# Kernel optimization log

Measured on AMD Instinct MI355X. Metric: run time of the kernel, lower is better.

Reference implementation:

```python
import jax, jax.numpy as jnp
import numpy as np

N, E, IN_DIM, OUT_DIM, SEM_DIM = 50000, 800000, 128, 128, 128
EPS = 1e-8


def setup_inputs() -> dict:
    key = jax.random.key(0)
    k = jax.random.split(key, 8)
    x = jax.random.normal(k[0], (N, IN_DIM), dtype=jnp.float32)
    edge_index = jax.random.randint(k[1], (2, E), 0, N, dtype=jnp.int64)
    semantic_vec = jax.random.normal(k[2], (N, SEM_DIM), dtype=jnp.float32)
    s = 1.0 / np.sqrt(IN_DIM)
    W_src = jax.random.uniform(k[3], (OUT_DIM, IN_DIM), jnp.float32, -s, s)
    b_src = jax.random.uniform(k[4], (OUT_DIM,), jnp.float32, -s, s)
    W_dst = jax.random.uniform(k[5], (OUT_DIM, IN_DIM), jnp.float32, -s, s)
    b_dst = jax.random.uniform(k[6], (OUT_DIM,), jnp.float32, -s, s)
    return {"x": x, "edge_index": edge_index, "semantic_vec": semantic_vec,
            "W_src": W_src, "b_src": b_src, "W_dst": W_dst, "b_dst": b_dst}


def _scatter_softmax(sim, dst, num_segments):
    # numerically stable segment-wise softmax over edges grouped by dst
    seg_max = jax.ops.segment_max(sim, dst, num_segments=num_segments)
    seg_max = jnp.where(jnp.isneginf(seg_max), 0.0, seg_max)
    e = jnp.exp(sim - seg_max[dst])
    seg_sum = jax.ops.segment_sum(e, dst, num_segments=num_segments)
    return e / (seg_sum[dst] + 1e-16)


def reference(x, edge_index, semantic_vec, W_src, b_src, W_dst, b_dst):
    src, dst = edge_index[0], edge_index[1]
    x_j = x[src] @ W_src.T + b_src           # [E, out_dim]
    # cosine similarity with torch eps semantics
    a = semantic_vec[src]
    b = semantic_vec[dst]
    na = jnp.maximum(jnp.linalg.norm(a, axis=-1), EPS)
    nb = jnp.maximum(jnp.linalg.norm(b, axis=-1), EPS)
    sim = jnp.sum(a * b, axis=-1) / (na * nb)  # [E]
    attn = _scatter_softmax(sim, dst, x.shape[0])
    msg = attn[:, None] * x_j                 # [E, out_dim]
    out = jax.ops.segment_sum(msg, dst, num_segments=x.shape[0])
    return out
```

## Files before the change

### kernel.cpp

```cpp
#include <hip/hip_runtime.h>
#include <hip/hip_fp16.h>

#define Nn 50000
#define Ee 800000
#define D  128
#define SLOT 64

#define B_SCAT 782
#define B_NORM 3125

struct h4 { __half2 lo, hi; };

typedef _Float16 f16x8 __attribute__((ext_vector_type(8)));
typedef float    f32x4 __attribute__((ext_vector_type(4)));

__global__ __launch_bounds__(256) void k_gemm(const float* __restrict__ x,
                                              const float* __restrict__ W,
                                              const float* __restrict__ b,
                                              __half* __restrict__ y16,
                                              int* __restrict__ cnt) {
  __shared__ __half sW16[128 * 136] __attribute__((aligned(16)));
  __shared__ __half sA16[64 * 136]  __attribute__((aligned(16)));
  int bid = blockIdx.x, tid = threadIdx.x;
  int n0 = bid * 64;

  if (tid < 16) {
    int idx = bid * 64 + tid * 4;
    *(int4*)(cnt + idx) = (int4){0, 0, 0, 0};
  }

  for (int r = 0; r < 16; r++) {
    int i = tid + 256 * r;
    int row = i >> 5, c4 = (i & 31) << 2;
    float4 w = *(const float4*)(W + (size_t)row * 128 + c4);
    __half2* dst = (__half2*)&sW16[row * 136 + c4];
    dst[0] = __floats2half2_rn(w.x, w.y);
    dst[1] = __floats2half2_rn(w.z, w.w);
  }
  for (int r = 0; r < 8; r++) {
    int i = tid + 256 * r;
    int row = i >> 5, c4 = (i & 31) << 2;
    int nr = n0 + row; if (nr >= Nn) nr = Nn - 1;
    float4 v = *(const float4*)(x + (size_t)nr * 128 + c4);
    __half2* dst = (__half2*)&sA16[row * 136 + c4];
    dst[0] = __floats2half2_rn(v.x, v.y);
    dst[1] = __floats2half2_rn(v.z, v.w);
  }
  __syncthreads();

  int wave = tid >> 6, lane = tid & 63;
  int g = lane >> 4, n16 = lane & 15;
  int m0 = n0 + wave * 16;

  f32x4 acc[8];
#pragma unroll
  for (int jt = 0; jt < 8; jt++) {
    float bias = b[jt * 16 + n16];
    acc[jt] = (f32x4){bias, bias, bias, bias};
  }

#pragma unroll
  for (int kt = 0; kt < 4; kt++) {
    f16x8 a = *(const f16x8*)(&sA16[(wave * 16 + n16) * 136 + kt * 32 + g * 8]);
#pragma unroll
    for (int jt = 0; jt < 8; jt++) {
      f16x8 bf = *(const f16x8*)(&sW16[(jt * 16 + n16) * 136 + kt * 32 + g * 8]);
      acc[jt] = __builtin_amdgcn_mfma_f32_16x16x32_f16(a, bf, acc[jt], 0, 0, 0);
    }
  }

#pragma unroll
  for (int jt = 0; jt < 8; jt++) {
#pragma unroll
    for (int r = 0; r < 4; r++) {
      int row = m0 + g * 4 + r;
      if (row < Nn)
        y16[(size_t)row * 128 + jt * 16 + n16] = __float2half(acc[jt][r]);
    }
  }
}

__global__ __launch_bounds__(256) void k_prep2(const int* __restrict__ ei,
                                               const float* __restrict__ sem,
                                               __half* __restrict__ sem16,
                                               int* __restrict__ cnt,
                                               unsigned short* __restrict__ slot16) {
  int bid = blockIdx.x, tid = threadIdx.x;
  if (bid < B_SCAT) {
    int base = bid * 1024 + tid;
#pragma unroll
    for (int u = 0; u < 4; u++) {
      int e = base + u * 256;
      if (e < Ee) {
        int s = ei[e], d = ei[Ee + e];
        int pos = atomicAdd(cnt + d, 1);
        if (pos < SLOT)
          slot16[(size_t)d * SLOT + pos] = (unsigned short)s;
      }
    }
  } else {
    int nb = (bid - B_SCAT) * 16;
    int wave = tid >> 6, lane = tid & 63;
#pragma unroll
    for (int it = 0; it < 4; it++) {
      int n = nb + it * 4 + wave;
      const float2 v = *(const float2*)(sem + (size_t)n * D + 2 * lane);
      float p = v.x * v.x + v.y * v.y;
#pragma unroll
      for (int off = 32; off > 0; off >>= 1) p += __shfl_xor(p, off);
      float inv = 1.0f / fmaxf(sqrtf(p), 1e-8f);
      *(__half2*)(sem16 + (size_t)n * D + 2 * lane) = __floats2half2_rn(v.x * inv, v.y * inv);
    }
  }
}

__global__ __launch_bounds__(256) void k_fused(const __half* __restrict__ sem16,
                                               const __half* __restrict__ y16,
                                               const unsigned short* __restrict__ slot16,
                                               const int* __restrict__ cnt,
                                               float* __restrict__ out) {
  int d = (blockIdx.x * 256 + threadIdx.x) >> 6;
  int lane = threadIdx.x & 63;
  if (d >= Nn) return;
  int sub = lane >> 5, l32 = lane & 31;
  int c = cnt[d]; if (c > SLOT) c = SLOT;

  int sv = (lane < c) ? (int)slot16[(size_t)d * SLOT + lane] : 0;

  h4 dref = ((const h4*)(sem16 + (size_t)d * D))[l32];
  float2 d0 = __half22float2(dref.lo), d1 = __half22float2(dref.hi);

  float Sp = 0.0f;
  float o0 = 0, o1 = 0, o2 = 0, o3 = 0;
  for (int i = 0; i < c; i += 4) {
    int ia = i + sub, ib = i + 2 + sub;
    int ca = ia < c ? ia : c - 1, cb = ib < c ? ib : c - 1;
    int sa = __shfl(sv, ca), sb = __shfl(sv, cb);
    h4 ra = ((const h4*)(sem16 + (size_t)sa * D))[l32];
    h4 rb = ((const h4*)(sem16 + (size_t)sb * D))[l32];
    h4 ya = ((const h4*)(y16 + (size_t)sa * D))[l32];
    h4 yb = ((const h4*)(y16 + (size_t)sb * D))[l32];
    float2 ra0 = __half22float2(ra.lo), ra1 = __half22float2(ra.hi);
    float2 rb0 = __half22float2(rb.lo), rb1 = __half22float2(rb.hi);
    float pa = d0.x * ra0.x + d0.y * ra0.y + d1.x * ra1.x + d1.y * ra1.y;
    float pb = d0.x * rb0.x + d0.y * rb0.y + d1.x * rb1.x + d1.y * rb1.y;
#pragma unroll
    for (int o = 16; o > 0; o >>= 1) { pa += __shfl_xor(pa, o); pb += __shfl_xor(pb, o); }
    float ea = __expf(pa); if (ia >= c) ea = 0.0f;
    float eb = __expf(pb); if (ib >= c) eb = 0.0f;
    Sp += ea + eb;
    float2 a0 = __half22float2(ya.lo), a1 = __half22float2(ya.hi);
    float2 b0 = __half22float2(yb.lo), b1 = __half22float2(yb.hi);
    o0 += ea * a0.x + eb * b0.x;
    o1 += ea * a0.y + eb * b0.y;
    o2 += ea * a1.x + eb * b1.x;
    o3 += ea * a1.y + eb * b1.y;
  }
  Sp += __shfl_xor(Sp, 32);
  o0 += __shfl_xor(o0, 32); o1 += __shfl_xor(o1, 32);
  o2 += __shfl_xor(o2, 32); o3 += __shfl_xor(o3, 32);
  if (sub == 0) {
    float inv = 1.0f / (Sp + 1e-16f);
    float4 r; r.x = o0 * inv; r.y = o1 * inv; r.z = o2 * inv; r.w = o3 * inv;
    *(float4*)(out + (size_t)d * D + l32 * 4) = r;
  }
}

extern "C" void kernel_launch(void* const* d_in, const int* in_sizes, int n_in,
                              void* d_out, int out_size, void* d_ws, size_t ws_size,
                              hipStream_t stream) {
  const float* x     = (const float*)d_in[0];
  const int*   ei    = (const int*)d_in[1];
  const float* sem   = (const float*)d_in[2];
  const float* W_src = (const float*)d_in[3];
  const float* b_src = (const float*)d_in[4];
  float* out = (float*)d_out;

  char* ws = (char*)d_ws;
  const size_t O_Y    = 0;
  const size_t O_S16  = 12800000;
  const size_t O_CNT  = 25600000;
  const size_t O_SS   = 25804800;
  const size_t NEED   = 32204800;
  if (ws_size < NEED) return;

  __half* y16   = (__half*)(ws + O_Y);
  __half* sem16 = (__half*)(ws + O_S16);
  int* cnt = (int*)(ws + O_CNT);
  unsigned short* slot16 = (unsigned short*)(ws + O_SS);

  k_gemm<<<(Nn + 63) / 64, 256, 0, stream>>>(x, W_src, b_src, y16, cnt);
  k_prep2<<<B_SCAT + B_NORM, 256, 0, stream>>>(ei, sem, sem16, cnt, slot16);
  k_fused<<<(Nn + 3) / 4, 256, 0, stream>>>(sem16, y16, slot16, cnt, out);
}
```

Before: 212.6 us.

## Interleave normalized semantics and projected features into one blob and merge prep kernels

Stores the normalized fp16 semantic row and the fp16 projected feature row side by side in one 512-byte blob per node, so each gathered neighbor takes a single contiguous region. The GEMM, scatter and norm kernels are merged into one launch, and counters are cleared with a memset. In the gather kernel, each 16-lane group now handles one edge with 8-wide fp16 loads and fdot2 dot products, four edges per iteration. This costs more cross-lane reductions at the end, and the d>=Nn guard was dropped, which is safe only because Nn is divisible by 4.

Result: no change. 216.8 us (+2.0%).

```diff
diff --git a/kernel.cpp b/kernel.cpp
--- a/kernel.cpp
+++ b/kernel.cpp
@@ -7,85 +7,25 @@
 #define SLOT 64
 
 #define B_SCAT 782
+#define B_GEMM 782
 #define B_NORM 3125
 
-struct h4 { __half2 lo, hi; };
-
 typedef _Float16 f16x8 __attribute__((ext_vector_type(8)));
+typedef _Float16 h2    __attribute__((ext_vector_type(2)));
 typedef float    f32x4 __attribute__((ext_vector_type(4)));
 
-__global__ __launch_bounds__(256) void k_gemm(const float* __restrict__ x,
-                                              const float* __restrict__ W,
-                                              const float* __restrict__ b,
-                                              __half* __restrict__ y16,
-                                              int* __restrict__ cnt) {
+
+__global__ __launch_bounds__(256) void k_pre(const float* __restrict__ x,
+                                             const float* __restrict__ W,
+                                             const float* __restrict__ b,
+                                             const int* __restrict__ ei,
+                                             const float* __restrict__ sem,
+                                             __half* __restrict__ blob,
+                                             int* __restrict__ cnt,
+                                             unsigned short* __restrict__ slot16) {
   __shared__ __half sW16[128 * 136] __attribute__((aligned(16)));
-  __shared__ __half sA16[64 * 136]  __attribute__((aligned(16)));
   int bid = blockIdx.x, tid = threadIdx.x;
-  int n0 = bid * 64;
 
-  if (tid < 16) {
-    int idx = bid * 64 + tid * 4;
-    *(int4*)(cnt + idx) = (int4){0, 0, 0, 0};
-  }
-
-  for (int r = 0; r < 16; r++) {
-    int i = tid + 256 * r;
-    int row = i >> 5, c4 = (i & 31) << 2;
-    float4 w = *(const float4*)(W + (size_t)row * 128 + c4);
-    __half2* dst = (__half2*)&sW16[row * 136 + c4];
-    dst[0] = __floats2half2_rn(w.x, w.y);
-    dst[1] = __floats2half2_rn(w.z, w.w);
-  }
-  for (int r = 0; r < 8; r++) {
-    int i = tid + 256 * r;
-    int row = i >> 5, c4 = (i & 31) << 2;
-    int nr = n0 + row; if (nr >= Nn) nr = Nn - 1;
-    float4 v = *(const float4*)(x + (size_t)nr * 128 + c4);
-    __half2* dst = (__half2*)&sA16[row * 136 + c4];
-    dst[0] = __floats2half2_rn(v.x, v.y);
-    dst[1] = __floats2half2_rn(v.z, v.w);
-  }
-  __syncthreads();
-
-  int wave = tid >> 6, lane = tid & 63;
-  int g = lane >> 4, n16 = lane & 15;
-  int m0 = n0 + wave * 16;
-
-  f32x4 acc[8];
-#pragma unroll
-  for (int jt = 0; jt < 8; jt++) {
-    float bias = b[jt * 16 + n16];
-    acc[jt] = (f32x4){bias, bias, bias, bias};
-  }
-
-#pragma unroll
-  for (int kt = 0; kt < 4; kt++) {
-    f16x8 a = *(const f16x8*)(&sA16[(wave * 16 + n16) * 136 + kt * 32 + g * 8]);
-#pragma unroll
-    for (int jt = 0; jt < 8; jt++) {
-      f16x8 bf = *(const f16x8*)(&sW16[(jt * 16 + n16) * 136 + kt * 32 + g * 8]);
-      acc[jt] = __builtin_amdgcn_mfma_f32_16x16x32_f16(a, bf, acc[jt], 0, 0, 0);
-    }
-  }
-
-#pragma unroll
-  for (int jt = 0; jt < 8; jt++) {
-#pragma unroll
-    for (int r = 0; r < 4; r++) {
-      int row = m0 + g * 4 + r;
-      if (row < Nn)
-        y16[(size_t)row * 128 + jt * 16 + n16] = __float2half(acc[jt][r]);
-    }
-  }
-}
-
-__global__ __launch_bounds__(256) void k_prep2(const int* __restrict__ ei,
-                                               const float* __restrict__ sem,
-                                               __half* __restrict__ sem16,
-                                               int* __restrict__ cnt,
-                                               unsigned short* __restrict__ slot16) {
-  int bid = blockIdx.x, tid = threadIdx.x;
   if (bid < B_SCAT) {
     int base = bid * 1024 + tid;
 #pragma unroll
@@ -98,8 +38,62 @@
           slot16[(size_t)d * SLOT + pos] = (unsigned short)s;
       }
     }
+  } else if (bid < B_SCAT + B_GEMM) {
+    int gb = bid - B_SCAT;
+    int n0 = gb * 64;
+
+    for (int r = 0; r < 16; r++) {
+      int i = tid + 256 * r;
+      int row = i >> 5, c4 = (i & 31) << 2;
+      float4 w = *(const float4*)(W + (size_t)row * 128 + c4);
+      __half2* dst = (__half2*)&sW16[row * 136 + c4];
+      dst[0] = __floats2half2_rn(w.x, w.y);
+      dst[1] = __floats2half2_rn(w.z, w.w);
+    }
+
+    int wave = tid >> 6, lane = tid & 63;
+    int g = lane >> 4, n16 = lane & 15;
+    int m0 = n0 + wave * 16;
+
+    int arow = m0 + n16; if (arow >= Nn) arow = Nn - 1;
+    const float* xr = x + (size_t)arow * 128 + g * 8;
+    union { f16x8 v; __half2 h[4]; } af[4];
+#pragma unroll
+    for (int kt = 0; kt < 4; kt++) {
+      float4 u = *(const float4*)(xr + kt * 32);
+      float4 q = *(const float4*)(xr + kt * 32 + 4);
+      af[kt].h[0] = __floats2half2_rn(u.x, u.y);
+      af[kt].h[1] = __floats2half2_rn(u.z, u.w);
+      af[kt].h[2] = __floats2half2_rn(q.x, q.y);
+      af[kt].h[3] = __floats2half2_rn(q.z, q.w);
+    }
+    __syncthreads();
+
+    f32x4 acc[8];
+#pragma unroll
+    for (int jt = 0; jt < 8; jt++) {
+      float bias = b[jt * 16 + n16];
+      acc[jt] = (f32x4){bias, bias, bias, bias};
+    }
+#pragma unroll
+    for (int kt = 0; kt < 4; kt++) {
+#pragma unroll
+      for (int jt = 0; jt < 8; jt++) {
+        f16x8 bf = *(const f16x8*)(&sW16[(jt * 16 + n16) * 136 + kt * 32 + g * 8]);
+        acc[jt] = __builtin_amdgcn_mfma_f32_16x16x32_f16(af[kt].v, bf, acc[jt], 0, 0, 0);
+      }
+    }
+#pragma unroll
+    for (int jt = 0; jt < 8; jt++) {
+#pragma unroll
+      for (int r = 0; r < 4; r++) {
+        int row = m0 + g * 4 + r;
+        if (row < Nn)
+          blob[(size_t)row * 256 + 128 + jt * 16 + n16] = __float2half(acc[jt][r]);
+      }
+    }
   } else {
-    int nb = (bid - B_SCAT) * 16;
+    int nb = (bid - B_SCAT - B_GEMM) * 16;
     int wave = tid >> 6, lane = tid & 63;
 #pragma unroll
     for (int it = 0; it < 4; it++) {
@@ -109,60 +103,61 @@
 #pragma unroll
       for (int off = 32; off > 0; off >>= 1) p += __shfl_xor(p, off);
       float inv = 1.0f / fmaxf(sqrtf(p), 1e-8f);
-      *(__half2*)(sem16 + (size_t)n * D + 2 * lane) = __floats2half2_rn(v.x * inv, v.y * inv);
+      *(__half2*)(blob + (size_t)n * 256 + 2 * lane) = __floats2half2_rn(v.x * inv, v.y * inv);
     }
   }
 }
 
-__global__ __launch_bounds__(256) void k_fused(const __half* __restrict__ sem16,
-                                               const __half* __restrict__ y16,
+__global__ __launch_bounds__(256) void k_fused(const __half* __restrict__ blob,
                                                const unsigned short* __restrict__ slot16,
                                                const int* __restrict__ cnt,
                                                float* __restrict__ out) {
   int d = (blockIdx.x * 256 + threadIdx.x) >> 6;
   int lane = threadIdx.x & 63;
-  if (d >= Nn) return;
-  int sub = lane >> 5, l32 = lane & 31;
+  int g = lane >> 4, l16 = lane & 15;
   int c = cnt[d]; if (c > SLOT) c = SLOT;
 
   int sv = (lane < c) ? (int)slot16[(size_t)d * SLOT + lane] : 0;
 
-  h4 dref = ((const h4*)(sem16 + (size_t)d * D))[l32];
-  float2 d0 = __half22float2(dref.lo), d1 = __half22float2(dref.hi);
+  f16x8 dh = *(const f16x8*)(blob + (size_t)d * 256 + l16 * 8);
 
+  float o[8] = {0, 0, 0, 0, 0, 0, 0, 0};
   float Sp = 0.0f;
-  float o0 = 0, o1 = 0, o2 = 0, o3 = 0;
+
   for (int i = 0; i < c; i += 4) {
-    int ia = i + sub, ib = i + 2 + sub;
-    int ca = ia < c ? ia : c - 1, cb = ib < c ? ib : c - 1;
-    int sa = __shfl(sv, ca), sb = __shfl(sv, cb);
-    h4 ra = ((const h4*)(sem16 + (size_t)sa * D))[l32];
-    h4 rb = ((const h4*)(sem16 + (size_t)sb * D))[l32];
-    h4 ya = ((const h4*)(y16 + (size_t)sa * D))[l32];
-    h4 yb = ((const h4*)(y16 + (size_t)sb * D))[l32];
-    float2 ra0 = __half22float2(ra.lo), ra1 = __half22float2(ra.hi);
-    float2 rb0 = __half22float2(rb.lo), rb1 = __half22float2(rb.hi);
-    float pa = d0.x * ra0.x + d0.y * ra0.y + d1.x * ra1.x + d1.y * ra1.y;
-    float pb = d0.x * rb0.x + d0.y * rb0.y + d1.x * rb1.x + d1.y * rb1.y;
+    int e = i + g;
+    int ce = e < c ? e : c - 1;
+    int sa = __shfl(sv, ce);
+    const __half* nbp = blob + (size_t)sa * 256;
+    f16x8 rs = *(const f16x8*)(nbp + l16 * 8);
+    f16x8 ry = *(const f16x8*)(nbp + 128 + l16 * 8);
+    float p = __builtin_amdgcn_fdot2((h2){rs[0], rs[1]}, (h2){dh[0], dh[1]}, 0.0f, false);
+    p = __builtin_amdgcn_fdot2((h2){rs[2], rs[3]}, (h2){dh[2], dh[3]}, p, false);
+    p = __builtin_amdgcn_fdot2((h2){rs[4], rs[5]}, (h2){dh[4], dh[5]}, p, false);
+    p = __builtin_amdgcn_fdot2((h2){rs[6], rs[7]}, (h2){dh[6], dh[7]}, p, false);
+    p += __shfl_xor(p, 1); p += __shfl_xor(p, 2);
+    p += __shfl_xor(p, 4); p += __shfl_xor(p, 8);
+    float ew = __expf(p); if (e >= c) ew = 0.0f;
+    Sp += ew;
 #pragma unroll
-    for (int o = 16; o > 0; o >>= 1) { pa += __shfl_xor(pa, o); pb += __shfl_xor(pb, o); }
-    float ea = __expf(pa); if (ia >= c) ea = 0.0f;
-    float eb = __expf(pb); if (ib >= c) eb = 0.0f;
-    Sp += ea + eb;
-    float2 a0 = __half22float2(ya.lo), a1 = __half22float2(ya.hi);
-    float2 b0 = __half22float2(yb.lo), b1 = __half22float2(yb.hi);
-    o0 += ea * a0.x + eb * b0.x;
-    o1 += ea * a0.y + eb * b0.y;
-    o2 += ea * a1.x + eb * b1.x;
-    o3 += ea * a1.y + eb * b1.y;
+    for (int k = 0; k < 8; k++) o[k] += ew * (float)ry[k];
   }
+
+#pragma unroll
+  for (int k = 0; k < 8; k++) {
+    o[k] += __shfl_xor(o[k], 16);
+    o[k] += __shfl_xor(o[k], 32);
+  }
+  Sp += __shfl_xor(Sp, 16);
   Sp += __shfl_xor(Sp, 32);
-  o0 += __shfl_xor(o0, 32); o1 += __shfl_xor(o1, 32);
-  o2 += __shfl_xor(o2, 32); o3 += __shfl_xor(o3, 32);
-  if (sub == 0) {
+
+  if (g == 0) {
     float inv = 1.0f / (Sp + 1e-16f);
-    float4 r; r.x = o0 * inv; r.y = o1 * inv; r.z = o2 * inv; r.w = o3 * inv;
-    *(float4*)(out + (size_t)d * D + l32 * 4) = r;
+    float4 r0; r0.x = o[0] * inv; r0.y = o[1] * inv; r0.z = o[2] * inv; r0.w = o[3] * inv;
+    float4 r1; r1.x = o[4] * inv; r1.y = o[5] * inv; r1.z = o[6] * inv; r1.w = o[7] * inv;
+    float* op = out + (size_t)d * D + l16 * 8;
+    *(float4*)op = r0;
+    *(float4*)(op + 4) = r1;
   }
 }
 
@@ -177,19 +172,18 @@
   float* out = (float*)d_out;
 
   char* ws = (char*)d_ws;
-  const size_t O_Y    = 0;
-  const size_t O_S16  = 12800000;
+  const size_t O_BLOB = 0;
   const size_t O_CNT  = 25600000;
   const size_t O_SS   = 25804800;
   const size_t NEED   = 32204800;
   if (ws_size < NEED) return;
 
-  __half* y16   = (__half*)(ws + O_Y);
-  __half* sem16 = (__half*)(ws + O_S16);
+  __half* blob = (__half*)(ws + O_BLOB);
   int* cnt = (int*)(ws + O_CNT);
   unsigned short* slot16 = (unsigned short*)(ws + O_SS);
 
-  k_gemm<<<(Nn + 63) / 64, 256, 0, stream>>>(x, W_src, b_src, y16, cnt);
-  k_prep2<<<B_SCAT + B_NORM, 256, 0, stream>>>(ei, sem, sem16, cnt, slot16);
-  k_fused<<<(Nn + 3) / 4, 256, 0, stream>>>(sem16, y16, slot16, cnt, out);
+  hipMemsetAsync(cnt, 0, 50048 * sizeof(int), stream);
+  k_pre<<<B_SCAT + B_GEMM + B_NORM, 256, 0, stream>>>(x, W_src, b_src, ei, sem,
+                                                      blob, cnt, slot16);
+  k_fused<<<(Nn + 3) / 4, 256, 0, stream>>>(blob, slot16, cnt, out);
 }
```
